# Performance work log

Measured on AMD Instinct MI355X. Metric: run time of the kernel, lower is better.

## Reference

```python
import jax, jax.numpy as jnp
import numpy as np

B, W, C, N = 2, 2048, 512, 8
K = C // N                      # 64
HALF = K * (K + 1) // 2 - K     # strict upper-triangle count
EPS = 1e-5


def _layernorm(x, gamma, beta):
    mu = jnp.mean(x, axis=-1, keepdims=True)
    var = jnp.mean(jnp.square(x - mu), axis=-1, keepdims=True)
    return (x - mu) * jax.lax.rsqrt(var + EPS) * gamma + beta


def _build_metric(halves, diagonals):
    # symmetric per-head metric: strict upper triangle from `halves`,
    # mirrored, diagonal overwritten by `diagonals` (diag of m+m^T is 0).
    iu0, iu1 = np.triu_indices(K, k=1)
    m = jnp.zeros((N, K, K), dtype=halves.dtype).at[:, iu0, iu1].set(halves)
    m = m + jnp.swapaxes(m, -1, -2)
    d = np.arange(K)
    return m.at[:, d, d].set(diagonals)


def setup_inputs() -> dict:
    key = jax.random.key(0)
    ks = jax.random.split(key, 9)
    return {
        "x1": jax.random.normal(ks[0], (B, W, C), jnp.float32),
        "x2": jax.random.normal(ks[1], (B, W, C), jnp.float32),
        "gamma": jnp.ones((C,), jnp.float32),
        "beta": jnp.zeros((C,), jnp.float32),
        "proj_nck": jax.random.normal(ks[2], (N, C, K), jnp.float32) * (C ** -0.5),
        "halves": jax.random.normal(ks[3], (N, HALF), jnp.float32) * 0.05,
        "diagonals": jax.random.normal(ks[4], (N, K), jnp.float32) * 0.05,
        "W_mixer": jax.random.normal(ks[5], (C, C), jnp.float32) * 0.02,
        "b_mixer": jnp.zeros((C,), jnp.float32),
    }


def reference(x1, x2, gamma, beta, proj_nck, halves, diagonals, W_mixer, b_mixer):
    x1n = _layernorm(x1, gamma, beta)
    x2n = _layernorm(x2, gamma, beta)
    metric_nkk = _build_metric(halves, diagonals)

    # per-head projections (same projection used for both sequences)
    p1_bnwk = jnp.einsum("bwc,nck->bnwk", x1n, proj_nck)
    p2_bnwk = jnp.einsum("bwc,nck->bnwk", x2n, proj_nck)

    # bilinear metric scores  Q . M . K^T  -> [B, N, W, W]
    dots_bnww = jnp.einsum("bnwk,nkj,bnvj->bnwv", p1_bnwk, metric_nkk, p2_bnwk)

    # NOTE: the original computes a scaled/masked softmax of dots_bnww but
    # never uses it for the output; the value mix uses the RAW dot products.
    # We omit the dead softmax — output math is identical.

    nudged_bnwk = jnp.einsum("bnwv,bnvk->bnwk", dots_bnww, p1_bnwk)
    nudged_bwc = jnp.transpose(nudged_bnwk, (0, 2, 1, 3)).reshape(x1.shape[0], x1.shape[1], C)
    return nudged_bwc @ W_mixer.T + b_mixer
```

## Files before the change

kernel.cpp:

```cpp
#include <hip/hip_runtime.h>

typedef unsigned short u16;
typedef __attribute__((ext_vector_type(8))) short short8;
typedef __attribute__((ext_vector_type(4))) float f32x4;

#define HALFN 2016

__device__ __forceinline__ u16 f2b_rn(float x) {
    union { float f; unsigned u; } v; v.f = x;
    unsigned r = v.u + 0x7FFFu + ((v.u >> 16) & 1u);
    return (u16)(r >> 16);
}

__device__ __forceinline__ void gll16(const void* g, void* s) {
    __builtin_amdgcn_global_load_lds(
        (const __attribute__((address_space(1))) unsigned int*)g,
        (__attribute__((address_space(3))) unsigned int*)s, 16, 0, 0);
}

__global__ __launch_bounds__(256) void ln_prep(const float* __restrict__ x1,
                                               const float* __restrict__ x2,
                                               const float* __restrict__ gamma,
                                               const float* __restrict__ beta,
                                               const float* __restrict__ proj,
                                               u16* __restrict__ Xh,
                                               u16* __restrict__ Pwh,
                                               float* __restrict__ S) {
    const int bid = blockIdx.x, t = threadIdx.x;

    if (bid < 2048) {
        const int wv = t >> 6, lane = t & 63;
        const int row = bid * 4 + wv;
        const float* src = (row < 4096) ? (x1 + (size_t)row * 512)
                                        : (x2 + (size_t)(row - 4096) * 512);
        float4 v0 = *(const float4*)&src[lane * 4];
        float4 v1 = *(const float4*)&src[256 + lane * 4];
        float s  = v0.x + v0.y + v0.z + v0.w + v1.x + v1.y + v1.z + v1.w;
        float sq = v0.x * v0.x + v0.y * v0.y + v0.z * v0.z + v0.w * v0.w +
                   v1.x * v1.x + v1.y * v1.y + v1.z * v1.z + v1.w * v1.w;
        #pragma unroll
        for (int off = 32; off > 0; off >>= 1) {
            s  += __shfl_down(s, off);
            sq += __shfl_down(sq, off);
        }
        s  = __shfl(s, 0);
        sq = __shfl(sq, 0);
        float mu  = s * (1.0f / 512.0f);
        float var = sq * (1.0f / 512.0f) - mu * mu;
        float rs  = rsqrtf(var + 1e-5f);
        float4 g0 = *(const float4*)&gamma[lane * 4];
        float4 g1 = *(const float4*)&gamma[256 + lane * 4];
        float4 b0 = *(const float4*)&beta[lane * 4];
        float4 b1 = *(const float4*)&beta[256 + lane * 4];
        ushort4 h0, h1;
        h0.x = f2b_rn((v0.x - mu) * rs * g0.x + b0.x);
        h0.y = f2b_rn((v0.y - mu) * rs * g0.y + b0.y);
        h0.z = f2b_rn((v0.z - mu) * rs * g0.z + b0.z);
        h0.w = f2b_rn((v0.w - mu) * rs * g0.w + b0.w);
        h1.x = f2b_rn((v1.x - mu) * rs * g1.x + b1.x);
        h1.y = f2b_rn((v1.y - mu) * rs * g1.y + b1.y);
        h1.z = f2b_rn((v1.z - mu) * rs * g1.z + b1.z);
        h1.w = f2b_rn((v1.w - mu) * rs * g1.w + b1.w);
        *(ushort4*)&Xh[(size_t)row * 512 + lane * 4] = h0;
        *(ushort4*)&Xh[(size_t)row * 512 + 256 + lane * 4] = h1;
    } else if (bid < 2112) {
        __shared__ float tile[64][65];
        const int id = bid - 2048;
        const int n = id >> 3, c0 = (id & 7) * 64;
        #pragma unroll
        for (int i = 0; i < 4; i++) {
            int flat = i * 256 + t;
            int c = flat >> 4, k4 = (flat & 15) * 4;
            float4 v = *(const float4*)&proj[(size_t)n * 32768 + (size_t)(c0 + c) * 64 + k4];
            tile[c][k4 + 0] = v.x; tile[c][k4 + 1] = v.y;
            tile[c][k4 + 2] = v.z; tile[c][k4 + 3] = v.w;
        }
        __syncthreads();
        #pragma unroll
        for (int i = 0; i < 16; i++) {
            int flat = i * 256 + t;
            int k = flat >> 6, c = flat & 63;
            Pwh[(size_t)(n * 64 + k) * 512 + c0 + c] = f2b_rn(tile[c][k]);
        }
    } else {
        float4 z = {0.f, 0.f, 0.f, 0.f};
        #pragma unroll
        for (int i = 0; i < 64; i++)
            *(float4*)&S[(size_t)(i * 256 + t) * 4] = z;
    }
}

__global__ __launch_bounds__(256) void proj_g_mfma(const u16* __restrict__ Xh,
                                                   const u16* __restrict__ Pwh,
                                                   u16* __restrict__ PPh,
                                                   float* __restrict__ S) {
    __shared__ u16 lds[24576];
    const int bx = blockIdx.x;
    const int n  = blockIdx.y;
    const int b = bx >> 5, v0 = (bx & 31) * 64;
    const u16* A1 = Xh + (size_t)(b * 2048 + v0) * 512;
    const u16* A2 = A1 + (size_t)4096 * 512;
    const u16* Bp = Pwh + (size_t)(n * 64) * 512;

    const int t = threadIdx.x, lane = t & 63, w = t >> 6, wm = w & 1, wn = w >> 1;
    const int fr = lane & 15, q = lane >> 4;

    int aoff[2][2], boff[2][2];
    #pragma unroll
    for (int kc = 0; kc < 2; kc++) {
        #pragma unroll
        for (int i = 0; i < 2; i++) {
            int r = wm * 32 + i * 16 + fr;
            aoff[kc][i] = r * 64 + (((kc * 4 + q) ^ (r & 7)) * 8);
        }
        #pragma unroll
        for (int j = 0; j < 2; j++) {
            int r = wn * 32 + j * 16 + fr;
            boff[kc][j] = r * 64 + (((kc * 4 + q) ^ (r & 7)) * 8);
        }
    }

    auto stage = [&](int kt, u16* buf) {
        #pragma unroll
        for (int p = 0; p < 2; p++) {
            int o = p * 4096 + t * 16;
            int r = o >> 7;
            int c = ((o >> 4) & 7) ^ (r & 7);
            size_t g = (size_t)r * 512 + kt + c * 8;
            gll16(A1 + g, buf + (o >> 1));
            gll16(A2 + g, buf + 4096 + (o >> 1));
            gll16(Bp + g, buf + 8192 + (o >> 1));
        }
    };

    f32x4 acc1[2][2] = {}, acc2[2][2] = {};
    stage(0, lds);
    __syncthreads();
    for (int k = 0; k < 8; k++) {
        u16* cur = lds + (k & 1) * 12288;
        if (k < 7) stage((k + 1) * 64, lds + ((k & 1) ^ 1) * 12288);
        #pragma unroll
        for (int kc = 0; kc < 2; kc++) {
            short8 a1f[2], a2f[2], bf[2];
            #pragma unroll
            for (int i = 0; i < 2; i++) {
                a1f[i] = *(const short8*)(cur + aoff[kc][i]);
                a2f[i] = *(const short8*)(cur + 4096 + aoff[kc][i]);
            }
            #pragma unroll
            for (int j = 0; j < 2; j++)
                bf[j] = *(const short8*)(cur + 8192 + boff[kc][j]);
            #pragma unroll
            for (int i = 0; i < 2; i++)
                #pragma unroll
                for (int j = 0; j < 2; j++) {
                    acc1[i][j] = __builtin_amdgcn_mfma_f32_16x16x32_bf16(a1f[i], bf[j], acc1[i][j], 0, 0, 0);
                    acc2[i][j] = __builtin_amdgcn_mfma_f32_16x16x32_bf16(a2f[i], bf[j], acc2[i][j], 0, 0, 0);
                }
        }
        __syncthreads();
    }

    #pragma unroll
    for (int i = 0; i < 2; i++) {
        const int mloc = wm * 32 + i * 16 + q * 4;
        #pragma unroll
        for (int j = 0; j < 2; j++) {
            const int c = wn * 32 + j * 16 + fr;
            u16 h1[4], h2[4];
            #pragma unroll
            for (int r = 0; r < 4; r++) {
                h1[r] = f2b_rn(acc1[i][j][r]);
                h2[r] = f2b_rn(acc2[i][j][r]);
            }
            #pragma unroll
            for (int r = 0; r < 4; r++)
                PPh[(size_t)(b * 2048 + v0 + mloc + r) * 512 + n * 64 + c] = h1[r];
            const int sw = c * 64 + (((mloc >> 3) ^ (c & 7)) * 8) + (mloc & 7);
            ushort4 u1; u1.x = h1[0]; u1.y = h1[1]; u1.z = h1[2]; u1.w = h1[3];
            ushort4 u2; u2.x = h2[0]; u2.y = h2[1]; u2.z = h2[2]; u2.w = h2[3];
            *(ushort4*)&lds[sw] = u1;
            *(ushort4*)&lds[4096 + sw] = u2;
        }
    }
    __syncthreads();

    f32x4 accg[2][2] = {};
    #pragma unroll
    for (int ks = 0; ks < 2; ks++) {
        short8 ag[2], bg[2];
        #pragma unroll
        for (int i = 0; i < 2; i++) {
            int jr = wm * 32 + i * 16 + fr;
            ag[i] = *(const short8*)&lds[4096 + jr * 64 + (((ks * 4 + q) ^ (jr & 7)) * 8)];
        }
        #pragma unroll
        for (int j = 0; j < 2; j++) {
            int kr = wn * 32 + j * 16 + fr;
            bg[j] = *(const short8*)&lds[kr * 64 + (((ks * 4 + q) ^ (kr & 7)) * 8)];
        }
        #pragma unroll
        for (int i = 0; i < 2; i++)
            #pragma unroll
            for (int j = 0; j < 2; j++)
                accg[i][j] = __builtin_amdgcn_mfma_f32_16x16x32_bf16(ag[i], bg[j], accg[i][j], 0, 0, 0);
    }
    float* Sb = S + (size_t)(b * 8 + n) * 4096;
    #pragma unroll
    for (int i = 0; i < 2; i++) {
        int jrow = wm * 32 + i * 16 + q * 4;
        #pragma unroll
        for (int j = 0; j < 2; j++) {
            int kk = wn * 32 + j * 16 + fr;
            #pragma unroll
            for (int r = 0; r < 4; r++)
                atomicAdd(&Sb[(jrow + r) * 64 + kk], accg[i][j][r]);
        }
    }
}

__global__ __launch_bounds__(256) void tu_kernel(const float* __restrict__ S,
                                                 const float* __restrict__ halves,
                                                 const float* __restrict__ diagonals,
                                                 const float* __restrict__ Wm,
                                                 u16* __restrict__ UTh) {
    __shared__ float Ms[64][65];
    __shared__ float Gs[64][68];
    __shared__ float Ts[64][68];
    const int bid = blockIdx.x, t = threadIdx.x;
    const int bn = bid >> 5, sub = bid & 31;
    const int b = bn >> 3, n = bn & 7;

    for (int idx = t; idx < 4096; idx += 256) {
        int r = idx >> 6, c = idx & 63;
        float val;
        if (r == c) {
            val = diagonals[n * 64 + r];
        } else {
            int rr = (r < c) ? r : c;
            int cc = (r < c) ? c : r;
            int h = rr * 63 - (rr * (rr - 1)) / 2 + (cc - rr - 1);
            val = halves[n * HALFN + h];
        }
        Ms[r][c] = val;
    }
    for (int idx = t; idx < 4096; idx += 256)
        Gs[idx >> 6][idx & 63] = S[(size_t)bn * 4096 + idx];
    __syncthreads();

    {
        const int k = t & 63, lq = t >> 6;
        float a[16] = {};
        for (int j = 0; j < 64; j++) {
            float m = Ms[k][j];
            const float* gp = &Gs[j][lq * 16];
            #pragma unroll
            for (int u4 = 0; u4 < 4; u4++) {
                float4 g4 = *(const float4*)&gp[u4 * 4];
                a[u4 * 4 + 0] = fmaf(m, g4.x, a[u4 * 4 + 0]);
                a[u4 * 4 + 1] = fmaf(m, g4.y, a[u4 * 4 + 1]);
                a[u4 * 4 + 2] = fmaf(m, g4.z, a[u4 * 4 + 2]);
                a[u4 * 4 + 3] = fmaf(m, g4.w, a[u4 * 4 + 3]);
            }
        }
        int pos = (lq ^ (k & 3)) * 16;
        #pragma unroll
        for (int u4 = 0; u4 < 4; u4++) {
            float4 v4 = {a[u4 * 4 + 0], a[u4 * 4 + 1], a[u4 * 4 + 2], a[u4 * 4 + 3]};
            *(float4*)&Ts[k][pos + u4 * 4] = v4;
        }
    }
    __syncthreads();

    const int k2 = t & 63, cgp = t >> 6;
    const int c0 = sub * 16 + cgp * 4;
    float uacc[4] = {};
    #pragma unroll
    for (int kkc = 0; kkc < 4; kkc++) {
        const float* tp = &Ts[k2][(kkc ^ (k2 & 3)) * 16];
        float ts[16];
        #pragma unroll
        for (int u = 0; u < 4; u++) {
            float4 t4 = *(const float4*)&tp[u * 4];
            ts[u * 4 + 0] = t4.x; ts[u * 4 + 1] = t4.y;
            ts[u * 4 + 2] = t4.z; ts[u * 4 + 3] = t4.w;
        }
        #pragma unroll
        for (int i = 0; i < 4; i++) {
            const float* wrow = &Wm[(size_t)(c0 + i) * 512 + n * 64 + kkc * 16];
            #pragma unroll
            for (int u = 0; u < 4; u++) {
                float4 w4 = *(const float4*)&wrow[u * 4];
                uacc[i] = fmaf(ts[u * 4 + 0], w4.x, uacc[i]);
                uacc[i] = fmaf(ts[u * 4 + 1], w4.y, uacc[i]);
                uacc[i] = fmaf(ts[u * 4 + 2], w4.z, uacc[i]);
                uacc[i] = fmaf(ts[u * 4 + 3], w4.w, uacc[i]);
            }
        }
    }
    #pragma unroll
    for (int i = 0; i < 4; i++)
        UTh[(size_t)b * 262144 + (size_t)(c0 + i) * 512 + n * 64 + k2] = f2b_rn(uacc[i]);
}

__global__ __launch_bounds__(256) void gemm_out_mfma(const u16* __restrict__ PPh,
                                                     const u16* __restrict__ UTh,
                                                     const float* __restrict__ bias,
                                                     float* __restrict__ out) {
    __shared__ u16 lds[16384];
    const int b = blockIdx.z;
    const u16* A  = PPh + (size_t)b * 2048 * 512;
    const u16* Bu = UTh + (size_t)b * 512 * 512;
    const int m0 = blockIdx.x * 64, n0 = blockIdx.y * 64;
    const int t = threadIdx.x, lane = t & 63, w = t >> 6, wm = w & 1, wn = w >> 1;
    const int fr = lane & 15, q = lane >> 4;

    int aoff[2][2], boff[2][2];
    #pragma unroll
    for (int kc = 0; kc < 2; kc++) {
        #pragma unroll
        for (int i = 0; i < 2; i++) {
            int r = wm * 32 + i * 16 + fr;
            aoff[kc][i] = r * 64 + (((kc * 4 + q) ^ (r & 7)) * 8);
        }
        #pragma unroll
        for (int j = 0; j < 2; j++) {
            int r = wn * 32 + j * 16 + fr;
            boff[kc][j] = r * 64 + (((kc * 4 + q) ^ (r & 7)) * 8);
        }
    }

    auto stage = [&](int kt, u16* buf) {
        #pragma unroll
        for (int p = 0; p < 2; p++) {
            int o = p * 4096 + t * 16;
            int r = o >> 7;
            int c = ((o >> 4) & 7) ^ (r & 7);
            gll16(A  + (size_t)(m0 + r) * 512 + kt + c * 8, buf + (o >> 1));
            gll16(Bu + (size_t)(n0 + r) * 512 + kt + c * 8, buf + 4096 + (o >> 1));
        }
    };

    f32x4 acc[2][2] = {};
    stage(0, lds);
    __syncthreads();
    for (int k = 0; k < 8; k++) {
        u16* cur = lds + (k & 1) * 8192;
        if (k < 7) stage((k + 1) * 64, lds + ((k & 1) ^ 1) * 8192);
        #pragma unroll
        for (int kc = 0; kc < 2; kc++) {
            short8 af[2], bf[2];
            #pragma unroll
            for (int i = 0; i < 2; i++)
                af[i] = *(const short8*)(cur + aoff[kc][i]);
            #pragma unroll
            for (int j = 0; j < 2; j++)
                bf[j] = *(const short8*)(cur + 4096 + boff[kc][j]);
            #pragma unroll
            for (int i = 0; i < 2; i++)
                #pragma unroll
                for (int j = 0; j < 2; j++)
                    acc[i][j] = __builtin_amdgcn_mfma_f32_16x16x32_bf16(af[i], bf[j], acc[i][j], 0, 0, 0);
        }
        __syncthreads();
    }

    #pragma unroll
    for (int i = 0; i < 2; i++) {
        int m = m0 + wm * 32 + i * 16 + q * 4;
        #pragma unroll
        for (int j = 0; j < 2; j++) {
            int n = n0 + wn * 32 + j * 16 + fr;
            float bv = bias[n];
            #pragma unroll
            for (int r = 0; r < 4; r++)
                out[(size_t)(b * 2048 + m + r) * 512 + n] = acc[i][j][r] + bv;
        }
    }
}

extern "C" void kernel_launch(void* const* d_in, const int* in_sizes, int n_in,
                              void* d_out, int out_size, void* d_ws, size_t ws_size,
                              hipStream_t stream) {
    (void)in_sizes; (void)n_in; (void)out_size; (void)ws_size;
    const float* x1        = (const float*)d_in[0];
    const float* x2        = (const float*)d_in[1];
    const float* gamma     = (const float*)d_in[2];
    const float* beta      = (const float*)d_in[3];
    const float* proj      = (const float*)d_in[4];
    const float* halves    = (const float*)d_in[5];
    const float* diagonals = (const float*)d_in[6];
    const float* Wm        = (const float*)d_in[7];
    const float* bmix      = (const float*)d_in[8];
    float* out = (float*)d_out;

    u16* us    = (u16*)d_ws;
    u16* Xh    = us;
    u16* Pwh   = Xh + 4194304;
    u16* PPh   = Pwh + 262144;
    u16* UTh   = PPh + 2097152;
    float* S   = (float*)(UTh + 524288);

    ln_prep<<<dim3(2113), 256, 0, stream>>>(x1, x2, gamma, beta, proj, Xh, Pwh, S);
    proj_g_mfma<<<dim3(64, 8), 256, 0, stream>>>(Xh, Pwh, PPh, S);
    tu_kernel<<<dim3(512), 256, 0, stream>>>(S, halves, diagonals, Wm, UTh);
    gemm_out_mfma<<<dim3(32, 8, 2), 256, 0, stream>>>(PPh, UTh, bmix, out);
}
```

Measured before the change: 116.7 us.

## Enlarge tiles: two heads per proj block, 128-row tiles in output GEMM

proj_g_mfma now handles two heads per block. Each wave pair takes one head, so the A tiles loaded from Xh are reused across both heads, and the grid shrinks from 64x8 to 64x4. gemm_out_mfma moves from 64x64 to 128x64 tiles, halving its block count and reusing each UTh tile across more rows. This cuts global and LDS traffic per FLOP, but uses more LDS and registers and leaves fewer blocks (256 each) to fill the 256 CUs of an MI355X.

```diff
diff --git a/kernel.cpp b/kernel.cpp
--- a/kernel.cpp
+++ b/kernel.cpp
@@ -94,18 +94,20 @@
                                                    const u16* __restrict__ Pwh,
                                                    u16* __restrict__ PPh,
                                                    float* __restrict__ S) {
-    __shared__ u16 lds[24576];
+    __shared__ u16 lds[2][16384];
     const int bx = blockIdx.x;
-    const int n  = blockIdx.y;
+    const int by = blockIdx.y;
     const int b = bx >> 5, v0 = (bx & 31) * 64;
+    const int h0 = by * 2;
     const u16* A1 = Xh + (size_t)(b * 2048 + v0) * 512;
     const u16* A2 = A1 + (size_t)4096 * 512;
-    const u16* Bp = Pwh + (size_t)(n * 64) * 512;
-
-    const int t = threadIdx.x, lane = t & 63, w = t >> 6, wm = w & 1, wn = w >> 1;
+    const u16* Bp = Pwh + (size_t)(h0 * 64) * 512;
+
+    const int t = threadIdx.x, lane = t & 63, w = t >> 6;
+    const int wm = w & 1, wh = w >> 1;
     const int fr = lane & 15, q = lane >> 4;
 
-    int aoff[2][2], boff[2][2];
+    int aoff[2][2], boff[2][4];
     #pragma unroll
     for (int kc = 0; kc < 2; kc++) {
         #pragma unroll
@@ -114,9 +116,9 @@
             aoff[kc][i] = r * 64 + (((kc * 4 + q) ^ (r & 7)) * 8);
         }
         #pragma unroll
-        for (int j = 0; j < 2; j++) {
-            int r = wn * 32 + j * 16 + fr;
-            boff[kc][j] = r * 64 + (((kc * 4 + q) ^ (r & 7)) * 8);
+        for (int j = 0; j < 4; j++) {
+            int r = wh * 64 + j * 16 + fr;
+            boff[kc][j] = 8192 + r * 64 + (((kc * 4 + q) ^ (r & 7)) * 8);
         }
     }
 
@@ -129,31 +131,37 @@
             size_t g = (size_t)r * 512 + kt + c * 8;
             gll16(A1 + g, buf + (o >> 1));
             gll16(A2 + g, buf + 4096 + (o >> 1));
-            gll16(Bp + g, buf + 8192 + (o >> 1));
+        }
+        #pragma unroll
+        for (int p = 0; p < 4; p++) {
+            int o = p * 4096 + t * 16;
+            int r = o >> 7;
+            int c = ((o >> 4) & 7) ^ (r & 7);
+            gll16(Bp + (size_t)r * 512 + kt + c * 8, buf + 8192 + (o >> 1));
         }
     };
 
-    f32x4 acc1[2][2] = {}, acc2[2][2] = {};
-    stage(0, lds);
+    f32x4 acc1[2][4] = {}, acc2[2][4] = {};
+    stage(0, lds[0]);
     __syncthreads();
     for (int k = 0; k < 8; k++) {
-        u16* cur = lds + (k & 1) * 12288;
-        if (k < 7) stage((k + 1) * 64, lds + ((k & 1) ^ 1) * 12288);
+        u16* cur = lds[k & 1];
+        if (k < 7) stage((k + 1) * 64, lds[(k & 1) ^ 1]);
         #pragma unroll
         for (int kc = 0; kc < 2; kc++) {
-            short8 a1f[2], a2f[2], bf[2];
+            short8 a1f[2], a2f[2], bf[4];
             #pragma unroll
             for (int i = 0; i < 2; i++) {
                 a1f[i] = *(const short8*)(cur + aoff[kc][i]);
                 a2f[i] = *(const short8*)(cur + 4096 + aoff[kc][i]);
             }
             #pragma unroll
-            for (int j = 0; j < 2; j++)
-                bf[j] = *(const short8*)(cur + 8192 + boff[kc][j]);
+            for (int j = 0; j < 4; j++)
+                bf[j] = *(const short8*)(cur + boff[kc][j]);
             #pragma unroll
             for (int i = 0; i < 2; i++)
                 #pragma unroll
-                for (int j = 0; j < 2; j++) {
+                for (int j = 0; j < 4; j++) {
                     acc1[i][j] = __builtin_amdgcn_mfma_f32_16x16x32_bf16(a1f[i], bf[j], acc1[i][j], 0, 0, 0);
                     acc2[i][j] = __builtin_amdgcn_mfma_f32_16x16x32_bf16(a2f[i], bf[j], acc2[i][j], 0, 0, 0);
                 }
@@ -165,8 +173,9 @@
     for (int i = 0; i < 2; i++) {
         const int mloc = wm * 32 + i * 16 + q * 4;
         #pragma unroll
-        for (int j = 0; j < 2; j++) {
-            const int c = wn * 32 + j * 16 + fr;
+        for (int j = 0; j < 4; j++) {
+            const int c = j * 16 + fr;
+            const int gcol = (h0 + wh) * 64 + c;
             u16 h1[4], h2[4];
             #pragma unroll
             for (int r = 0; r < 4; r++) {
@@ -175,43 +184,43 @@
             }
             #pragma unroll
             for (int r = 0; r < 4; r++)
-                PPh[(size_t)(b * 2048 + v0 + mloc + r) * 512 + n * 64 + c] = h1[r];
-            const int sw = c * 64 + (((mloc >> 3) ^ (c & 7)) * 8) + (mloc & 7);
+                PPh[(size_t)(b * 2048 + v0 + mloc + r) * 512 + gcol] = h1[r];
+            const int sw = wh * 8192 + c * 64 + (((mloc >> 3) ^ (c & 7)) * 8) + (mloc & 7);
             ushort4 u1; u1.x = h1[0]; u1.y = h1[1]; u1.z = h1[2]; u1.w = h1[3];
             ushort4 u2; u2.x = h2[0]; u2.y = h2[1]; u2.z = h2[2]; u2.w = h2[3];
-            *(ushort4*)&lds[sw] = u1;
-            *(ushort4*)&lds[4096 + sw] = u2;
+            *(ushort4*)&lds[0][sw] = u1;
+            *(ushort4*)&lds[0][4096 + sw] = u2;
         }
     }
     __syncthreads();
 
-    f32x4 accg[2][2] = {};
+    f32x4 accg[2][4] = {};
     #pragma unroll
     for (int ks = 0; ks < 2; ks++) {
-        short8 ag[2], bg[2];
+        short8 ag[2], bg[4];
         #pragma unroll
         for (int i = 0; i < 2; i++) {
             int jr = wm * 32 + i * 16 + fr;
-            ag[i] = *(const short8*)&lds[4096 + jr * 64 + (((ks * 4 + q) ^ (jr & 7)) * 8)];
-        }
-        #pragma unroll
-        for (int j = 0; j < 2; j++) {
-            int kr = wn * 32 + j * 16 + fr;
-            bg[j] = *(const short8*)&lds[kr * 64 + (((ks * 4 + q) ^ (kr & 7)) * 8)];
+            ag[i] = *(const short8*)&lds[0][wh * 8192 + 4096 + jr * 64 + (((ks * 4 + q) ^ (jr & 7)) * 8)];
+        }
+        #pragma unroll
+        for (int j = 0; j < 4; j++) {
+            int kr = j * 16 + fr;
+            bg[j] = *(const short8*)&lds[0][wh * 8192 + kr * 64 + (((ks * 4 + q) ^ (kr & 7)) * 8)];
         }
         #pragma unroll
         for (int i = 0; i < 2; i++)
             #pragma unroll
-            for (int j = 0; j < 2; j++)
+            for (int j = 0; j < 4; j++)
                 accg[i][j] = __builtin_amdgcn_mfma_f32_16x16x32_bf16(ag[i], bg[j], accg[i][j], 0, 0, 0);
     }
-    float* Sb = S + (size_t)(b * 8 + n) * 4096;
+    float* Sb = S + (size_t)(b * 8 + h0 + wh) * 4096;
     #pragma unroll
     for (int i = 0; i < 2; i++) {
         int jrow = wm * 32 + i * 16 + q * 4;
         #pragma unroll
-        for (int j = 0; j < 2; j++) {
-            int kk = wn * 32 + j * 16 + fr;
+        for (int j = 0; j < 4; j++) {
+            int kk = j * 16 + fr;
             #pragma unroll
             for (int r = 0; r < 4; r++)
                 atomicAdd(&Sb[(jrow + r) * 64 + kk], accg[i][j][r]);
@@ -307,57 +316,64 @@
                                                      const u16* __restrict__ UTh,
                                                      const float* __restrict__ bias,
                                                      float* __restrict__ out) {
-    __shared__ u16 lds[16384];
+    __shared__ u16 lds[2][12288];
     const int b = blockIdx.z;
     const u16* A  = PPh + (size_t)b * 2048 * 512;
     const u16* Bu = UTh + (size_t)b * 512 * 512;
-    const int m0 = blockIdx.x * 64, n0 = blockIdx.y * 64;
-    const int t = threadIdx.x, lane = t & 63, w = t >> 6, wm = w & 1, wn = w >> 1;
+    const int m0 = blockIdx.x * 128, n0 = blockIdx.y * 64;
+    const int t = threadIdx.x, lane = t & 63, w = t >> 6;
+    const int wm = w & 1, wn = w >> 1;
     const int fr = lane & 15, q = lane >> 4;
 
-    int aoff[2][2], boff[2][2];
+    int aoff[2][4], boff[2][2];
     #pragma unroll
     for (int kc = 0; kc < 2; kc++) {
         #pragma unroll
-        for (int i = 0; i < 2; i++) {
-            int r = wm * 32 + i * 16 + fr;
+        for (int i = 0; i < 4; i++) {
+            int r = wm * 64 + i * 16 + fr;
             aoff[kc][i] = r * 64 + (((kc * 4 + q) ^ (r & 7)) * 8);
         }
         #pragma unroll
         for (int j = 0; j < 2; j++) {
             int r = wn * 32 + j * 16 + fr;
-            boff[kc][j] = r * 64 + (((kc * 4 + q) ^ (r & 7)) * 8);
+            boff[kc][j] = 8192 + r * 64 + (((kc * 4 + q) ^ (r & 7)) * 8);
         }
     }
 
     auto stage = [&](int kt, u16* buf) {
+        #pragma unroll
+        for (int p = 0; p < 4; p++) {
+            int o = p * 4096 + t * 16;
+            int r = o >> 7;
+            int c = ((o >> 4) & 7) ^ (r & 7);
+            gll16(A + (size_t)(m0 + r) * 512 + kt + c * 8, buf + (o >> 1));
+        }
         #pragma unroll
         for (int p = 0; p < 2; p++) {
             int o = p * 4096 + t * 16;
             int r = o >> 7;
             int c = ((o >> 4) & 7) ^ (r & 7);
-            gll16(A  + (size_t)(m0 + r) * 512 + kt + c * 8, buf + (o >> 1));
-            gll16(Bu + (size_t)(n0 + r) * 512 + kt + c * 8, buf + 4096 + (o >> 1));
+            gll16(Bu + (size_t)(n0 + r) * 512 + kt + c * 8, buf + 8192 + (o >> 1));
         }
     };
 
-    f32x4 acc[2][2] = {};
-    stage(0, lds);
+    f32x4 acc[4][2] = {};
+    stage(0, lds[0]);
     __syncthreads();
     for (int k = 0; k < 8; k++) {
-        u16* cur = lds + (k & 1) * 8192;
-        if (k < 7) stage((k + 1) * 64, lds + ((k & 1) ^ 1) * 8192);
+        u16* cur = lds[k & 1];
+        if (k < 7) stage((k + 1) * 64, lds[(k & 1) ^ 1]);
         #pragma unroll
         for (int kc = 0; kc < 2; kc++) {
-            short8 af[2], bf[2];
-            #pragma unroll
-            for (int i = 0; i < 2; i++)
+            short8 af[4], bf[2];
+            #pragma unroll
+            for (int i = 0; i < 4; i++)
                 af[i] = *(const short8*)(cur + aoff[kc][i]);
             #pragma unroll
             for (int j = 0; j < 2; j++)
-                bf[j] = *(const short8*)(cur + 4096 + boff[kc][j]);
-            #pragma unroll
-            for (int i = 0; i < 2; i++)
+                bf[j] = *(const short8*)(cur + boff[kc][j]);
+            #pragma unroll
+            for (int i = 0; i < 4; i++)
                 #pragma unroll
                 for (int j = 0; j < 2; j++)
                     acc[i][j] = __builtin_amdgcn_mfma_f32_16x16x32_bf16(af[i], bf[j], acc[i][j], 0, 0, 0);
@@ -366,8 +382,8 @@
     }
 
     #pragma unroll
-    for (int i = 0; i < 2; i++) {
-        int m = m0 + wm * 32 + i * 16 + q * 4;
+    for (int i = 0; i < 4; i++) {
+        int m = m0 + wm * 64 + i * 16 + q * 4;
         #pragma unroll
         for (int j = 0; j < 2; j++) {
             int n = n0 + wn * 32 + j * 16 + fr;
@@ -402,7 +418,7 @@
     float* S   = (float*)(UTh + 524288);
 
     ln_prep<<<dim3(2113), 256, 0, stream>>>(x1, x2, gamma, beta, proj, Xh, Pwh, S);
-    proj_g_mfma<<<dim3(64, 8), 256, 0, stream>>>(Xh, Pwh, PPh, S);
+    proj_g_mfma<<<dim3(64, 4), 256, 0, stream>>>(Xh, Pwh, PPh, S);
     tu_kernel<<<dim3(512), 256, 0, stream>>>(S, halves, diagonals, Wm, UTh);
-    gemm_out_mfma<<<dim3(32, 8, 2), 256, 0, stream>>>(PPh, UTh, bmix, out);
-}
+    gemm_out_mfma<<<dim3(16, 8, 2), 256, 0, stream>>>(PPh, UTh, bmix, out);
+}
```

Result: slower. 121.2 us (+3.8%).
